# Kernel tuning notes

Hardware: AMD Instinct MI355X
Metric: run time of the kernel (lower is better)

Reference implementation:

```python
import jax, jax.numpy as jnp
import numpy as np
from jax import lax

B, DIM, H, W = 8, 256, 48, 48
HEADS, DH = 8, 32
K, S = 5, 2
P = K // 2
SCALE = DH ** -0.5
EPS = 1e-5


def setup_inputs() -> dict:
    key = jax.random.key(0)
    ks = jax.random.split(key, 12)
    w = lambda k, sh: jax.random.normal(k, sh, jnp.float32) * 0.02
    return {
        'x': jax.random.normal(ks[0], (B, DIM, H, W), jnp.float32),
        'kv': jax.random.normal(ks[1], (B, DIM, H, W), jnp.float32),
        'wq': w(ks[2], (DIM, DIM)), 'bq': jnp.zeros((DIM,), jnp.float32),
        'wk': w(ks[3], (DIM, DIM)), 'bk': jnp.zeros((DIM,), jnp.float32),
        'wv': w(ks[4], (DIM, DIM)), 'bv': jnp.zeros((DIM,), jnp.float32),
        'w_dw': w(ks[5], (DH, 1, K, K)), 'b_dw': jnp.zeros((DH,), jnp.float32),
        'ln_w': jnp.ones((DH,), jnp.float32), 'ln_b': jnp.zeros((DH,), jnp.float32),
        'w_off': w(ks[6], (2, DH)),
        'wo': w(ks[7], (DIM, DIM)), 'bo': jnp.zeros((DIM,), jnp.float32),
    }


def conv1x1(x, w, b=None):
    # x: (B, Cin, H, W), w: (Cout, Cin)
    y = jnp.einsum('oc,bchw->bohw', w, x)
    return y if b is None else y + b[None, :, None, None]


def grid_sample_bilinear(inp, grid):
    # inp: (N, C, Hh, Ww); grid: (N, Hg, Wg, 2) in (x, y), align_corners=True
    N, C, Hh, Ww = inp.shape
    gx = (grid[..., 0] + 1.0) * 0.5 * (Ww - 1)
    gy = (grid[..., 1] + 1.0) * 0.5 * (Hh - 1)
    x0 = jnp.floor(gx)
    y0 = jnp.floor(gy)
    wx = gx - x0  # frac weights for x1/y1 corners
    wy = gy - y0
    x0i = jnp.clip(x0.astype(jnp.int32), 0, Ww - 1)
    x1i = jnp.clip(x0.astype(jnp.int32) + 1, 0, Ww - 1)
    y0i = jnp.clip(y0.astype(jnp.int32), 0, Hh - 1)
    y1i = jnp.clip(y0.astype(jnp.int32) + 1, 0, Hh - 1)
    flat = inp.reshape(N, C, Hh * Ww)
    n = grid.shape[1] * grid.shape[2]

    def gather(yi, xi):
        idx = (yi * Ww + xi).reshape(N, 1, n)
        return jnp.take_along_axis(flat, jnp.broadcast_to(idx, (N, C, n)), axis=2)

    w00 = ((1 - wx) * (1 - wy)).reshape(N, 1, n)
    w01 = (wx * (1 - wy)).reshape(N, 1, n)
    w10 = ((1 - wx) * wy).reshape(N, 1, n)
    w11 = (wx * wy).reshape(N, 1, n)
    return (w00 * gather(y0i, x0i) + w01 * gather(y0i, x1i)
            + w10 * gather(y1i, x0i) + w11 * gather(y1i, x1i))  # (N, C, n)


def reference(x, kv, wq, bq, wk, bk, wv, bv, w_dw, b_dw, ln_w, ln_b, w_off, wo, bo):
    q = conv1x1(x, wq, bq)                      # (B, DIM, H, W)
    q_off = q.reshape(B * HEADS, DH, H, W)      # per-head channels
    # depthwise offset conv
    t = lax.conv_general_dilated(q_off, w_dw, (S, S), [(P, P), (P, P)],
                                 feature_group_count=DH,
                                 dimension_numbers=('NCHW', 'OIHW', 'NCHW'))
    t = t + b_dw[None, :, None, None]
    Hk, Wk = t.shape[2], t.shape[3]
    n = Hk * Wk
    # LayerNormProxy: LN over channel dim
    t = t.transpose(0, 2, 3, 1)                 # (BH, Hk, Wk, DH)
    mu = t.mean(-1, keepdims=True)
    var = ((t - mu) ** 2).mean(-1, keepdims=True)
    t = (t - mu) / jnp.sqrt(var + EPS) * ln_w + ln_b
    t = jax.nn.gelu(t, approximate=False)
    offset = jnp.einsum('oc,bhwc->bhwo', w_off, t)  # (BH, Hk, Wk, 2) as (y, x)
    # reference points, normalized to [-1, 1]
    ref_y = (jnp.linspace(0.5, Hk - 0.5, Hk, dtype=jnp.float32) / (Hk - 1.0)) * 2.0 - 1.0
    ref_x = (jnp.linspace(0.5, Wk - 0.5, Wk, dtype=jnp.float32) / (Wk - 1.0)) * 2.0 - 1.0
    ref = jnp.stack(jnp.meshgrid(ref_y, ref_x, indexing='ij'), axis=-1)  # (Hk, Wk, 2)
    pos = jnp.clip(offset + ref[None], -1.0, 1.0)
    grid = pos[..., ::-1]                       # (x, y) order for sampling
    kvs = grid_sample_bilinear(kv.reshape(B * HEADS, DH, H, W), grid)  # (BH, DH, n)
    kv4 = kvs.reshape(B, DIM, 1, n)
    k = conv1x1(kv4, wk, bk).reshape(B * HEADS, DH, n)
    v = conv1x1(kv4, wv, bv).reshape(B * HEADS, DH, n)
    qf = q.reshape(B * HEADS, DH, H * W)
    attn = jax.nn.softmax(jnp.einsum('bcm,bcn->bmn', qf, k) * SCALE, axis=2)
    out = jnp.einsum('bmn,bcn->bcm', attn, v).reshape(B, DIM, H, W)
    return conv1x1(out, wo, bo)
```

## Files before the change

kernel.cpp:

```cpp
#include <hip/hip_runtime.h>
#include <hip/hip_bf16.h>
#include <cstddef>

#define BB 8
#define DIM 256
#define HH 48
#define WW 48
#define HW 2304
#define HEADS 8
#define DH 32
#define BH 64
#define HK 24
#define WK 24
#define NN 576
#define SCALE 0.17677669529663687f
#define EPSF 1e-5f

typedef __attribute__((ext_vector_type(8))) short short8;
typedef __attribute__((ext_vector_type(4))) float f32x4;

static __device__ inline short f2bf_s(float f) {
  __hip_bfloat16 h = __float2bfloat16(f);
  return *reinterpret_cast<short*>(&h);
}

static __device__ inline unsigned pkrnd(float a, float b) {
  unsigned ua = __builtin_bit_cast(unsigned, a) + 0x8000u;
  unsigned ub = __builtin_bit_cast(unsigned, b) + 0x8000u;
  return __builtin_amdgcn_perm(ub, ua, 0x07060302);
}

__global__ __launch_bounds__(256) void prep(
    const float* __restrict__ x, const float* __restrict__ wq,
    short* __restrict__ Xh, short* __restrict__ Xl,
    short* __restrict__ Wqh, short* __restrict__ Wql) {
  __shared__ float t[64][65];
  const int bid = blockIdx.x;
  if (bid < 1152) {
    int mt = bid % 36, t2 = bid / 36;
    int ct = t2 & 3, b = t2 >> 2;
    const int c0 = ct * 64, m0 = mt * 64;
    const int col = threadIdx.x & 63, row4 = threadIdx.x >> 6;
    const float* xb = x + ((size_t)b * 256 + c0) * HW + m0;
#pragma unroll
    for (int k = 0; k < 16; k++) {
      int c = row4 + k * 4;
      t[c][col] = xb[(size_t)c * HW + col];
    }
    __syncthreads();
    short* oh = Xh + ((size_t)b * HW + m0) * 256 + c0;
    short* ol = Xl + ((size_t)b * HW + m0) * 256 + c0;
#pragma unroll
    for (int k = 0; k < 16; k++) {
      int m = row4 + k * 4;
      float v = t[col][m];
      unsigned u = __builtin_bit_cast(unsigned, v) & 0xffff0000u;
      float rem = v - __builtin_bit_cast(float, u);
      oh[(size_t)m * 256 + col] = (short)(u >> 16);
      ol[(size_t)m * 256 + col] = (short)(__builtin_bit_cast(unsigned, rem) >> 16);
    }
  } else {
    int e0 = (bid - 1152) * 1024 + threadIdx.x * 4;
    float4 v4 = *(const float4*)(wq + e0);
    float vv[4] = {v4.x, v4.y, v4.z, v4.w};
    union { short s[4]; int2 i2; } Hu, Lu;
#pragma unroll
    for (int j = 0; j < 4; j++) {
      unsigned u = __builtin_bit_cast(unsigned, vv[j]) & 0xffff0000u;
      float rem = vv[j] - __builtin_bit_cast(float, u);
      Hu.s[j] = (short)(u >> 16);
      Lu.s[j] = (short)(__builtin_bit_cast(unsigned, rem) >> 16);
    }
    *(int2*)(Wqh + e0) = Hu.i2;
    *(int2*)(Wql + e0) = Lu.i2;
  }
}

__global__ __launch_bounds__(512) void gemm_q_fused(
    const short* __restrict__ Wh, const short* __restrict__ Wl,
    const float* __restrict__ bias,
    const short* __restrict__ Xh, const short* __restrict__ Xl,
    float* __restrict__ Y,
    const float* __restrict__ kv, float* __restrict__ kvT,
    const float* __restrict__ wk, const float* __restrict__ wv,
    const float* __restrict__ wo,
    short* __restrict__ Wkh, short* __restrict__ Wkl,
    short* __restrict__ Wvh, short* __restrict__ Wvl,
    short* __restrict__ Woh, short* __restrict__ Wol) {
  __shared__ short sB[2][64 * 256];
  const int bid = blockIdx.x;
  const int tid = threadIdx.x;

  if (bid < 288) {
    const int b = bid / 36;
    const int mBase = (bid % 36) * 64;
    const short* srcH = Xh + ((size_t)b * HW + mBase) * 256;
    const short* srcL = Xl + ((size_t)b * HW + mBase) * 256;
#pragma unroll
    for (int it = 0; it < 4; it++) {
      int idx = it * 512 + tid;
      int row = idx >> 5, ck = idx & 31;
      int dst = row * 256 + ((ck ^ (row & 7)) << 3);
      *(short8*)(&sB[0][dst]) = *(const short8*)(srcH + (size_t)row * 256 + ck * 8);
      *(short8*)(&sB[1][dst]) = *(const short8*)(srcL + (size_t)row * 256 + ck * 8);
    }
    __syncthreads();

    const int wave = tid >> 6, lane = tid & 63;
    const int quad = lane >> 4, l15 = lane & 15;
    const int oBase = wave * 32;
    f32x4 acc[2][4] = {};
    for (int kc = 0; kc < 256; kc += 32) {
      short8 ah[2], al[2];
#pragma unroll
      for (int os = 0; os < 2; os++) {
        ah[os] = *(const short8*)(Wh + (size_t)(oBase + os * 16 + l15) * 256 + kc + quad * 8);
        al[os] = *(const short8*)(Wl + (size_t)(oBase + os * 16 + l15) * 256 + kc + quad * 8);
      }
#pragma unroll
      for (int mt = 0; mt < 4; mt++) {
        int row = mt * 16 + l15;
        int off = row * 256 + ((((kc >> 3) + quad) ^ (row & 7)) << 3);
        short8 bh_ = *(const short8*)(&sB[0][off]);
        short8 bl_ = *(const short8*)(&sB[1][off]);
#pragma unroll
        for (int os = 0; os < 2; os++) {
          acc[os][mt] = __builtin_amdgcn_mfma_f32_16x16x32_bf16(ah[os], bh_, acc[os][mt], 0, 0, 0);
          acc[os][mt] = __builtin_amdgcn_mfma_f32_16x16x32_bf16(al[os], bh_, acc[os][mt], 0, 0, 0);
          acc[os][mt] = __builtin_amdgcn_mfma_f32_16x16x32_bf16(ah[os], bl_, acc[os][mt], 0, 0, 0);
        }
      }
    }
#pragma unroll
    for (int os = 0; os < 2; os++)
#pragma unroll
      for (int r = 0; r < 4; r++) {
        int o = oBase + os * 16 + quad * 4 + r;
        float bs = bias[o];
        float* yp = Y + ((size_t)b * 256 + o) * HW + mBase + l15;
#pragma unroll
        for (int mt = 0; mt < 4; mt++) yp[mt * 16] = acc[os][mt][r] + bs;
      }
  } else if (bid < 1440) {
    float* tf = (float*)sB;
    int bb = bid - 288;
    int mt = bb % 36, t2 = bb / 36;
    int ct = t2 & 3, b = t2 >> 2;
    const int c0 = ct * 64, m0 = mt * 64;
    const int col = tid & 63, row8 = tid >> 6;
    const float* xb = kv + ((size_t)b * 256 + c0) * HW + m0;
#pragma unroll
    for (int k = 0; k < 8; k++) {
      int c = row8 + k * 8;
      tf[c * 65 + col] = xb[(size_t)c * HW + col];
    }
    __syncthreads();
    float* ot = kvT + ((size_t)b * HW + m0) * 256 + c0;
#pragma unroll
    for (int k = 0; k < 8; k++) {
      int m = row8 + k * 8;
      ot[(size_t)m * 256 + col] = tf[col * 65 + m];
    }
  } else {
    const float* srcs[3] = {wk, wv, wo};
    short* his[3] = {Wkh, Wvh, Woh};
    short* los[3] = {Wkl, Wvl, Wol};
    int bb = bid - 1440;
    int w = bb >> 5;
    int off = (bb & 31) * 2048 + tid * 4;
    float4 v4 = *(const float4*)(srcs[w] + off);
    float vv[4] = {v4.x, v4.y, v4.z, v4.w};
    union { short s[4]; int2 i2; } Hu, Lu;
#pragma unroll
    for (int j = 0; j < 4; j++) {
      unsigned u = __builtin_bit_cast(unsigned, vv[j]) & 0xffff0000u;
      float rem = vv[j] - __builtin_bit_cast(float, u);
      Hu.s[j] = (short)(u >> 16);
      Lu.s[j] = (short)(__builtin_bit_cast(unsigned, rem) >> 16);
    }
    *(int2*)(his[w] + off) = Hu.i2;
    *(int2*)(los[w] + off) = Lu.i2;
  }
}

#define QPS 101
__global__ __launch_bounds__(256) void dw_sample_kernel(
    const float* __restrict__ q, const float* __restrict__ kvT,
    const float* __restrict__ w_dw, const float* __restrict__ b_dw,
    const float* __restrict__ ln_w, const float* __restrict__ ln_b,
    const float* __restrict__ w_off, short* __restrict__ kvsTh,
    short* __restrict__ kvsTl) {
  __shared__ float s_q[32 * QPS];
  __shared__ float s_w[DH * 25];
  const int tid = threadIdx.x;
  const int ch = tid & 31;
  const int np = tid >> 5;
  const int bid = blockIdx.x;
  const int b = bid & 7;
  const int r = bid >> 3;
  const int head = r / 72;
  const int rr = r - head * 72;
  const int yk = rr / 3;
  const int xk0 = (rr - yk * 3) * 8;
  const int bh = b * 8 + head;
  const int xk = xk0 + np;
  const int n = yk * WK + xk;

  for (int i = tid; i < DH * 25; i += 256) s_w[i] = w_dw[i];

  {
    const int y0 = yk * 2 - 2, x0 = xk0 * 2 - 2;
    const float* qbh = q + (size_t)bh * DH * HW;
#pragma unroll
    for (int it = 0; it < 13; it++) {
      int e = it * 256 + tid;
      if (e < 3200) {
        int c = e / 100;
        int rem = e - c * 100;
        int dy = rem / 20;
        int xl = rem - dy * 20;
        int gy = y0 + dy, gx = x0 + xl;
        float v = 0.f;
        if ((unsigned)gy < HH && (unsigned)gx < WW)
          v = qbh[(size_t)c * HW + gy * WW + gx];
        s_q[c * QPS + dy * 20 + xl] = v;
      }
    }
  }
  __syncthreads();

  float t = b_dw[ch];
  {
    const float* wp = s_w + ch * 25;
    const float* qp = s_q + ch * QPS + np * 2;
#pragma unroll
    for (int dy = 0; dy < 5; dy++)
#pragma unroll
      for (int dx = 0; dx < 5; dx++)
        t += wp[dy * 5 + dx] * qp[dy * 20 + dx];
  }

  float mu = t;
#pragma unroll
  for (int m = 1; m < 32; m <<= 1) mu += __shfl_xor(mu, m);
  mu *= (1.0f / DH);
  float d = t - mu;
  float var = d * d;
#pragma unroll
  for (int m = 1; m < 32; m <<= 1) var += __shfl_xor(var, m);
  var *= (1.0f / DH);
  float rstd = rsqrtf(var + EPSF);

  float xn = d * rstd * ln_w[ch] + ln_b[ch];
  float g = 0.5f * xn * (1.0f + erff(xn * 0.70710678118654752f));
  float o0 = w_off[ch] * g;
  float o1 = w_off[DH + ch] * g;
#pragma unroll
  for (int m = 1; m < 32; m <<= 1) {
    o0 += __shfl_xor(o0, m);
    o1 += __shfl_xor(o1, m);
  }

  const float ref_y = (0.5f + (float)yk) / 23.0f * 2.0f - 1.0f;
  const float ref_x = (0.5f + (float)xk) / 23.0f * 2.0f - 1.0f;
  float py = fminf(fmaxf(o0 + ref_y, -1.0f), 1.0f);
  float px = fminf(fmaxf(o1 + ref_x, -1.0f), 1.0f);

  float gx = (px + 1.0f) * 0.5f * 47.0f;
  float gy = (py + 1.0f) * 0.5f * 47.0f;
  float x0f = floorf(gx), y0f = floorf(gy);
  float wx = gx - x0f, wy = gy - y0f;
  int x0 = (int)x0f, y0 = (int)y0f;
  int x0i = min(max(x0, 0), WW - 1);
  int x1i = min(max(x0 + 1, 0), WW - 1);
  int y0i = min(max(y0, 0), HH - 1);
  int y1i = min(max(y0 + 1, 0), HH - 1);
  float w00 = (1.f - wx) * (1.f - wy);
  float w01 = wx * (1.f - wy);
  float w10 = (1.f - wx) * wy;
  float w11 = wx * wy;

  const float* kvb = kvT + (size_t)b * HW * 256 + head * DH + ch;
  float val = w00 * kvb[(size_t)(y0i * WW + x0i) * 256]
            + w01 * kvb[(size_t)(y0i * WW + x1i) * 256]
            + w10 * kvb[(size_t)(y1i * WW + x0i) * 256]
            + w11 * kvb[(size_t)(y1i * WW + x1i) * 256];

  unsigned ub = __builtin_bit_cast(unsigned, val);
  unsigned uh = ub & 0xffff0000u;
  float rem = val - __builtin_bit_cast(float, uh);
  size_t idx = ((size_t)b * NN + n) * 256 + head * DH + ch;
  kvsTh[idx] = (short)(uh >> 16);
  kvsTl[idx] = (short)(__builtin_bit_cast(unsigned, rem) >> 16);
}

__global__ __launch_bounds__(256) void kv_gemm_mfma(
    const short* __restrict__ Wkh, const short* __restrict__ Wkl,
    const float* __restrict__ bk,
    const short* __restrict__ Wvh, const short* __restrict__ Wvl,
    const float* __restrict__ bv,
    const short* __restrict__ Xh, const short* __restrict__ Xl,
    short* __restrict__ Kb, short* __restrict__ Vb) {
  const int tid = threadIdx.x;
  const int wave = tid >> 6;
  const int lane = tid & 63;
  const int quad = lane >> 4, l15 = lane & 15;
  const int b = blockIdx.z;
  const int mode = blockIdx.y >> 2;
  const int oTile = (blockIdx.y & 3) * 64;
  const int nBase = blockIdx.x * 64;

  if (mode == 0) {
    const int nW = nBase + wave * 16;
    const short* arh = Xh + ((size_t)b * NN + nW + l15) * 256 + quad * 8;
    const short* arl = Xl + ((size_t)b * NN + nW + l15) * 256 + quad * 8;
    f32x4 acc[4] = {};
    for (int kc = 0; kc < 256; kc += 32) {
      short8 ah = *(const short8*)(arh + kc);
      short8 al = *(const short8*)(arl + kc);
#pragma unroll
      for (int ot = 0; ot < 4; ot++) {
        short8 bh_ = *(const short8*)(Wkh + (size_t)(oTile + ot * 16 + l15) * 256 + kc + quad * 8);
        short8 bl_ = *(const short8*)(Wkl + (size_t)(oTile + ot * 16 + l15) * 256 + kc + quad * 8);
        acc[ot] = __builtin_amdgcn_mfma_f32_16x16x32_bf16(ah, bh_, acc[ot], 0, 0, 0);
        acc[ot] = __builtin_amdgcn_mfma_f32_16x16x32_bf16(al, bh_, acc[ot], 0, 0, 0);
        acc[ot] = __builtin_amdgcn_mfma_f32_16x16x32_bf16(ah, bl_, acc[ot], 0, 0, 0);
      }
    }
    float bs[4];
#pragma unroll
    for (int ot = 0; ot < 4; ot++) bs[ot] = bk[oTile + ot * 16 + l15];
#pragma unroll
    for (int r = 0; r < 4; r++) {
      short* yp = Kb + ((size_t)b * NN + nW + quad * 4 + r) * 256 + oTile + l15;
#pragma unroll
      for (int ot = 0; ot < 4; ot++) yp[ot * 16] = f2bf_s(acc[ot][r] + bs[ot]);
    }
  } else {
    const int oW = oTile + wave * 16;
    const short* arh = Wvh + (size_t)(oW + l15) * 256 + quad * 8;
    const short* arl = Wvl + (size_t)(oW + l15) * 256 + quad * 8;
    f32x4 acc[4] = {};
    for (int kc = 0; kc < 256; kc += 32) {
      short8 ah = *(const short8*)(arh + kc);
      short8 al = *(const short8*)(arl + kc);
#pragma unroll
      for (int nt = 0; nt < 4; nt++) {
        short8 bh_ = *(const short8*)(Xh + ((size_t)b * NN + nBase + nt * 16 + l15) * 256 + kc + quad * 8);
        short8 bl_ = *(const short8*)(Xl + ((size_t)b * NN + nBase + nt * 16 + l15) * 256 + kc + quad * 8);
        acc[nt] = __builtin_amdgcn_mfma_f32_16x16x32_bf16(ah, bh_, acc[nt], 0, 0, 0);
        acc[nt] = __builtin_amdgcn_mfma_f32_16x16x32_bf16(al, bh_, acc[nt], 0, 0, 0);
        acc[nt] = __builtin_amdgcn_mfma_f32_16x16x32_bf16(ah, bl_, acc[nt], 0, 0, 0);
      }
    }
#pragma unroll
    for (int r = 0; r < 4; r++) {
      int o = oW + quad * 4 + r;
      float bs = bv[o];
      short* yp = Vb + ((size_t)b * 256 + o) * NN + nBase + l15;
#pragma unroll
      for (int nt = 0; nt < 4; nt++) yp[nt * 16] = f2bf_s(acc[nt][r] + bs);
    }
  }
}

__global__ __launch_bounds__(256) void attn_mfma(const float* __restrict__ q,
                                                 const short* __restrict__ Kb,
                                                 const short* __restrict__ Vb,
                                                 short* __restrict__ O) {
  __shared__ short sK[2][64 * 40];
  __shared__ short sV[2][32 * 88];
  __shared__ int sP[4][2][256];
  const int tid = threadIdx.x;
  const int wave = tid >> 6;
  const int lane = tid & 63;
  const int quad = lane >> 4;
  const int l15 = lane & 15;
  const int bh = blockIdx.y;
  const int b = bh >> 3, head = bh & 7;
  const int mBase = blockIdx.x * 128 + wave * 32;

  short8 bq[2];
#pragma unroll
  for (int mt = 0; mt < 2; mt++) {
    const float* qp = q + ((size_t)bh * DH + quad * 8) * HW + mBase + mt * 16 + l15;
    short8 v;
#pragma unroll
    for (int j = 0; j < 8; j++) v[j] = f2bf_s(qp[(size_t)j * HW] * SCALE);
    bq[mt] = v;
  }

  const int kn = tid >> 2, kc = (tid & 3) * 8;
  const int vc = tid >> 3, vn = (tid & 7) * 8;
  const short* kg = Kb + (size_t)b * NN * 256 + head * DH;
  const short* vg = Vb + ((size_t)b * 256 + head * DH) * NN;

  short8 kreg = *(const short8*)(kg + (size_t)kn * 256 + kc);
  short8 vreg = *(const short8*)(vg + (size_t)vc * NN + vn);
  *(short8*)(&sK[0][kn * 40 + kc]) = kreg;
  *(short8*)(&sV[0][vc * 88 + vn]) = vreg;
  __syncthreads();

  const int g = (l15 >> 1) & 3;
  const int row16 = l15 * 16;
  const int wr0 = row16 + (((quad >> 1) ^ g) << 2) + ((quad & 1) << 1);
  const int wr1 = row16 + (((2 + (quad >> 1)) ^ g) << 2) + ((quad & 1) << 1);
  const int rd = row16 + ((quad ^ g) << 2);

  f32x4 oacc[2][2] = {};
  f32x4 dacc[2] = {};
  const short ONE = 0x3F80;
  const short8 ones = {ONE, ONE, ONE, ONE, ONE, ONE, ONE, ONE};

  for (int s = 0; s < 9; s++) {
    const int buf = s & 1;
    if (s + 1 < 9) {
      kreg = *(const short8*)(kg + (size_t)((s + 1) * 64 + kn) * 256 + kc);
      vreg = *(const short8*)(vg + (size_t)vc * NN + (s + 1) * 64 + vn);
    }
#pragma unroll
    for (int nt = 0; nt < 2; nt++) {
      short8 ka0 = *(const short8*)(&sK[buf][(nt * 32 + l15) * 40 + quad * 8]);
      short8 ka1 = *(const short8*)(&sK[buf][(nt * 32 + 16 + l15) * 40 + quad * 8]);
      short8 va0 = *(const short8*)(&sV[buf][l15 * 88 + nt * 32 + quad * 8]);
      short8 va1 = *(const short8*)(&sV[buf][(16 + l15) * 88 + nt * 32 + quad * 8]);
      f32x4 z = {0.f, 0.f, 0.f, 0.f};
      f32x4 st[2][2];
      st[0][0] = __builtin_amdgcn_mfma_f32_16x16x32_bf16(ka0, bq[0], z, 0, 0, 0);
      st[0][1] = __builtin_amdgcn_mfma_f32_16x16x32_bf16(ka1, bq[0], z, 0, 0, 0);
      st[1][0] = __builtin_amdgcn_mfma_f32_16x16x32_bf16(ka0, bq[1], z, 0, 0, 0);
      st[1][1] = __builtin_amdgcn_mfma_f32_16x16x32_bf16(ka1, bq[1], z, 0, 0, 0);
#pragma unroll
      for (int mt = 0; mt < 2; mt++) {
        float p0 = __expf(st[mt][0][0]), p1 = __expf(st[mt][0][1]);
        float p2 = __expf(st[mt][0][2]), p3 = __expf(st[mt][0][3]);
        float p4 = __expf(st[mt][1][0]), p5 = __expf(st[mt][1][1]);
        float p6 = __expf(st[mt][1][2]), p7 = __expf(st[mt][1][3]);
        int* base = &sP[wave][mt][0];
        *(int2*)(base + wr0) = make_int2((int)pkrnd(p0, p1), (int)pkrnd(p2, p3));
        *(int2*)(base + wr1) = make_int2((int)pkrnd(p4, p5), (int)pkrnd(p6, p7));
      }
#pragma unroll
      for (int mt = 0; mt < 2; mt++) {
        short8 pa = *(short8*)(&sP[wave][mt][0] + rd);
        oacc[mt][0] = __builtin_amdgcn_mfma_f32_16x16x32_bf16(pa, va0, oacc[mt][0], 0, 0, 0);
        oacc[mt][1] = __builtin_amdgcn_mfma_f32_16x16x32_bf16(pa, va1, oacc[mt][1], 0, 0, 0);
        dacc[mt] = __builtin_amdgcn_mfma_f32_16x16x32_bf16(pa, ones, dacc[mt], 0, 0, 0);
      }
    }
    if (s + 1 < 9) {
      *(short8*)(&sK[buf ^ 1][kn * 40 + kc]) = kreg;
      *(short8*)(&sV[buf ^ 1][vc * 88 + vn]) = vreg;
    }
    __syncthreads();
  }

#pragma unroll
  for (int mt = 0; mt < 2; mt++) {
    short* ob = O + ((size_t)b * HW + mBase + mt * 16) * 256 + head * DH + l15;
#pragma unroll
    for (int r = 0; r < 4; r++) {
      float inv = 1.0f / dacc[mt][r];
      ob[(size_t)(quad * 4 + r) * 256] = f2bf_s(oacc[mt][0][r] * inv);
      ob[(size_t)(quad * 4 + r) * 256 + 16] = f2bf_s(oacc[mt][1][r] * inv);
    }
  }
}

__global__ __launch_bounds__(512) void wo_gemm_mfma(const short* __restrict__ Whi,
                                                    const short* __restrict__ Wlo,
                                                    const float* __restrict__ bias,
                                                    const short* __restrict__ X,
                                                    float* __restrict__ Y) {
  __shared__ short sX[64 * 256];
  const int tid = threadIdx.x;
  const int b = blockIdx.y;
  const int mBase = blockIdx.x * 64;

  const short* src = X + ((size_t)b * HW + mBase) * 256;
#pragma unroll
  for (int it = 0; it < 4; it++) {
    int idx = it * 512 + tid;
    int row = idx >> 5, ck = idx & 31;
    *(short8*)(&sX[row * 256 + ((ck ^ (row & 7)) << 3)]) =
        *(const short8*)(src + (size_t)row * 256 + ck * 8);
  }
  __syncthreads();

  const int wave = tid >> 6, lane = tid & 63;
  const int quad = lane >> 4, l15 = lane & 15;
  const int oBase = wave * 32;

  f32x4 acc[2][4] = {};
  for (int kc = 0; kc < 256; kc += 32) {
    short8 ah[2], al[2];
#pragma unroll
    for (int os = 0; os < 2; os++) {
      ah[os] = *(const short8*)(Whi + (size_t)(oBase + os * 16 + l15) * 256 + kc + quad * 8);
      al[os] = *(const short8*)(Wlo + (size_t)(oBase + os * 16 + l15) * 256 + kc + quad * 8);
    }
#pragma unroll
    for (int mt = 0; mt < 4; mt++) {
      int row = mt * 16 + l15;
      short8 bx = *(const short8*)(&sX[row * 256 + ((((kc >> 3) + quad) ^ (row & 7)) << 3)]);
#pragma unroll
      for (int os = 0; os < 2; os++) {
        acc[os][mt] = __builtin_amdgcn_mfma_f32_16x16x32_bf16(ah[os], bx, acc[os][mt], 0, 0, 0);
        acc[os][mt] = __builtin_amdgcn_mfma_f32_16x16x32_bf16(al[os], bx, acc[os][mt], 0, 0, 0);
      }
    }
  }

#pragma unroll
  for (int os = 0; os < 2; os++)
#pragma unroll
    for (int r = 0; r < 4; r++) {
      int o = oBase + os * 16 + quad * 4 + r;
      float bs = bias[o];
      float* yp = Y + ((size_t)b * 256 + o) * HW + mBase + l15;
#pragma unroll
      for (int mt = 0; mt < 4; mt++) yp[mt * 16] = acc[os][mt][r] + bs;
    }
}

extern "C" void kernel_launch(void* const* d_in, const int* in_sizes, int n_in,
                              void* d_out, int out_size, void* d_ws, size_t ws_size,
                              hipStream_t stream) {
  const float* x    = (const float*)d_in[0];
  const float* kv   = (const float*)d_in[1];
  const float* wq   = (const float*)d_in[2];
  const float* bq   = (const float*)d_in[3];
  const float* wk   = (const float*)d_in[4];
  const float* bk   = (const float*)d_in[5];
  const float* wv   = (const float*)d_in[6];
  const float* bv   = (const float*)d_in[7];
  const float* w_dw = (const float*)d_in[8];
  const float* b_dw = (const float*)d_in[9];
  const float* ln_w = (const float*)d_in[10];
  const float* ln_b = (const float*)d_in[11];
  const float* w_off= (const float*)d_in[12];
  const float* wo   = (const float*)d_in[13];
  const float* bo   = (const float*)d_in[14];
  float* out = (float*)d_out;
  float* ws = (float*)d_ws;

  float* q     = ws;
  short* Xth   = (short*)(ws + 4718592);
  short* O     = (short*)(ws + 4718592);
  short* Xtl   = (short*)(ws + 7077888);
  short* kvsTh = (short*)(ws + 7077888);
  short* kvsTl = (short*)(ws + 7667712);
  short* Kb    = (short*)(ws + 8257536);
  short* Vb    = (short*)(ws + 8847360);
  short* Wqh   = (short*)(ws + 9437184);
  short* Wql = Wqh + 65536;
  short* Wkh = Wql + 65536;
  short* Wkl = Wkh + 65536;
  short* Wvh = Wkl + 65536;
  short* Wvl = Wvh + 65536;
  short* Woh = Wvl + 65536;
  short* Wol = Woh + 65536;
  float* kvT = out;

  prep<<<dim3(1216), dim3(256), 0, stream>>>(x, wq, Xth, Xtl, Wqh, Wql);
  gemm_q_fused<<<dim3(1536), dim3(512), 0, stream>>>(
      Wqh, Wql, bq, Xth, Xtl, q,
      kv, kvT, wk, wv, wo, Wkh, Wkl, Wvh, Wvl, Woh, Wol);
  dw_sample_kernel<<<dim3(BH * NN / 8), dim3(256), 0, stream>>>(
      q, kvT, w_dw, b_dw, ln_w, ln_b, w_off, kvsTh, kvsTl);
  kv_gemm_mfma<<<dim3(NN / 64, 8, BB), dim3(256), 0, stream>>>(
      Wkh, Wkl, bk, Wvh, Wvl, bv, kvsTh, kvsTl, Kb, Vb);
  attn_mfma<<<dim3(HW / 128, BH), dim3(256), 0, stream>>>(q, Kb, Vb, O);
  wo_gemm_mfma<<<dim3(HW / 64, BB), dim3(512), 0, stream>>>(Woh, Wol, bo, O, out);
}
```

Baseline: 230.7 us.

## Retile Q/Wo GEMMs, emit pre-scaled bf16 Q, add MFMA priority hints

The Q-projection and output GEMMs now use 256-thread blocks over 32-row tiles, with each wave covering 64 output channels. This doubles the block count and is meant to improve occupancy and reuse of the weight fragments. The Q GEMM epilogue also writes a head-major, scale-folded bf16 copy of Q, so attention loads its Q fragments with two vector loads instead of strided fp32 reads and per-element conversion. The attention kernel wraps its MFMA groups in s_setprio, and the transpose and weight-split branches are remapped to the new block size. The cost is an extra bf16 Q buffer write and more per-wave accumulator registers.

```diff
diff --git a/kernel.cpp b/kernel.cpp
--- a/kernel.cpp
+++ b/kernel.cpp
@@ -76,29 +76,29 @@
   }
 }
 
-__global__ __launch_bounds__(512) void gemm_q_fused(
+__global__ __launch_bounds__(256) void gemm_q_fused(
     const short* __restrict__ Wh, const short* __restrict__ Wl,
     const float* __restrict__ bias,
     const short* __restrict__ Xh, const short* __restrict__ Xl,
-    float* __restrict__ Y,
+    float* __restrict__ Y, short* __restrict__ Qbf,
     const float* __restrict__ kv, float* __restrict__ kvT,
     const float* __restrict__ wk, const float* __restrict__ wv,
     const float* __restrict__ wo,
     short* __restrict__ Wkh, short* __restrict__ Wkl,
     short* __restrict__ Wvh, short* __restrict__ Wvl,
     short* __restrict__ Woh, short* __restrict__ Wol) {
-  __shared__ short sB[2][64 * 256];
+  __shared__ short sB[2][32 * 256];
   const int bid = blockIdx.x;
   const int tid = threadIdx.x;
 
-  if (bid < 288) {
-    const int b = bid / 36;
-    const int mBase = (bid % 36) * 64;
+  if (bid < 576) {
+    const int b = bid & 7;
+    const int mBase = (bid >> 3) * 32;
     const short* srcH = Xh + ((size_t)b * HW + mBase) * 256;
     const short* srcL = Xl + ((size_t)b * HW + mBase) * 256;
 #pragma unroll
     for (int it = 0; it < 4; it++) {
-      int idx = it * 512 + tid;
+      int idx = it * 256 + tid;
       int row = idx >> 5, ck = idx & 31;
       int dst = row * 256 + ((ck ^ (row & 7)) << 3);
       *(short8*)(&sB[0][dst]) = *(const short8*)(srcH + (size_t)row * 256 + ck * 8);
@@ -108,23 +108,23 @@
 
     const int wave = tid >> 6, lane = tid & 63;
     const int quad = lane >> 4, l15 = lane & 15;
-    const int oBase = wave * 32;
-    f32x4 acc[2][4] = {};
+    const int oBase = wave * 64;
+    f32x4 acc[4][2] = {};
     for (int kc = 0; kc < 256; kc += 32) {
-      short8 ah[2], al[2];
-#pragma unroll
-      for (int os = 0; os < 2; os++) {
+      short8 ah[4], al[4];
+#pragma unroll
+      for (int os = 0; os < 4; os++) {
         ah[os] = *(const short8*)(Wh + (size_t)(oBase + os * 16 + l15) * 256 + kc + quad * 8);
         al[os] = *(const short8*)(Wl + (size_t)(oBase + os * 16 + l15) * 256 + kc + quad * 8);
       }
 #pragma unroll
-      for (int mt = 0; mt < 4; mt++) {
+      for (int mt = 0; mt < 2; mt++) {
         int row = mt * 16 + l15;
         int off = row * 256 + ((((kc >> 3) + quad) ^ (row & 7)) << 3);
         short8 bh_ = *(const short8*)(&sB[0][off]);
         short8 bl_ = *(const short8*)(&sB[1][off]);
 #pragma unroll
-        for (int os = 0; os < 2; os++) {
+        for (int os = 0; os < 4; os++) {
           acc[os][mt] = __builtin_amdgcn_mfma_f32_16x16x32_bf16(ah[os], bh_, acc[os][mt], 0, 0, 0);
           acc[os][mt] = __builtin_amdgcn_mfma_f32_16x16x32_bf16(al[os], bh_, acc[os][mt], 0, 0, 0);
           acc[os][mt] = __builtin_amdgcn_mfma_f32_16x16x32_bf16(ah[os], bl_, acc[os][mt], 0, 0, 0);
@@ -132,42 +132,48 @@
       }
     }
 #pragma unroll
-    for (int os = 0; os < 2; os++)
+    for (int os = 0; os < 4; os++)
 #pragma unroll
       for (int r = 0; r < 4; r++) {
         int o = oBase + os * 16 + quad * 4 + r;
         float bs = bias[o];
+        int head = o >> 5, c = o & 31;
         float* yp = Y + ((size_t)b * 256 + o) * HW + mBase + l15;
-#pragma unroll
-        for (int mt = 0; mt < 4; mt++) yp[mt * 16] = acc[os][mt][r] + bs;
-      }
-  } else if (bid < 1440) {
+        short* qp = Qbf + ((size_t)(b * 8 + head) * HW + mBase + l15) * 32 + c;
+#pragma unroll
+        for (int mt = 0; mt < 2; mt++) {
+          float v = acc[os][mt][r] + bs;
+          yp[mt * 16] = v;
+          qp[mt * 16 * 32] = f2bf_s(v * SCALE);
+        }
+      }
+  } else if (bid < 1728) {
     float* tf = (float*)sB;
-    int bb = bid - 288;
+    int bb = bid - 576;
     int mt = bb % 36, t2 = bb / 36;
     int ct = t2 & 3, b = t2 >> 2;
     const int c0 = ct * 64, m0 = mt * 64;
-    const int col = tid & 63, row8 = tid >> 6;
+    const int col = tid & 63, row4 = tid >> 6;
     const float* xb = kv + ((size_t)b * 256 + c0) * HW + m0;
 #pragma unroll
-    for (int k = 0; k < 8; k++) {
-      int c = row8 + k * 8;
+    for (int k = 0; k < 16; k++) {
+      int c = row4 + k * 4;
       tf[c * 65 + col] = xb[(size_t)c * HW + col];
     }
     __syncthreads();
     float* ot = kvT + ((size_t)b * HW + m0) * 256 + c0;
 #pragma unroll
-    for (int k = 0; k < 8; k++) {
-      int m = row8 + k * 8;
+    for (int k = 0; k < 16; k++) {
+      int m = row4 + k * 4;
       ot[(size_t)m * 256 + col] = tf[col * 65 + m];
     }
   } else {
     const float* srcs[3] = {wk, wv, wo};
     short* his[3] = {Wkh, Wvh, Woh};
     short* los[3] = {Wkl, Wvl, Wol};
-    int bb = bid - 1440;
-    int w = bb >> 5;
-    int off = (bb & 31) * 2048 + tid * 4;
+    int bb = bid - 1728;
+    int w = bb >> 6;
+    int off = (bb & 63) * 1024 + tid * 4;
     float4 v4 = *(const float4*)(srcs[w] + off);
     float vv[4] = {v4.x, v4.y, v4.z, v4.w};
     union { short s[4]; int2 i2; } Hu, Lu;
@@ -364,7 +370,7 @@
   }
 }
 
-__global__ __launch_bounds__(256) void attn_mfma(const float* __restrict__ q,
+__global__ __launch_bounds__(256) void attn_mfma(const short* __restrict__ Qbf,
                                                  const short* __restrict__ Kb,
                                                  const short* __restrict__ Vb,
                                                  short* __restrict__ O) {
@@ -381,13 +387,10 @@
   const int mBase = blockIdx.x * 128 + wave * 32;
 
   short8 bq[2];
-#pragma unroll
-  for (int mt = 0; mt < 2; mt++) {
-    const float* qp = q + ((size_t)bh * DH + quad * 8) * HW + mBase + mt * 16 + l15;
-    short8 v;
-#pragma unroll
-    for (int j = 0; j < 8; j++) v[j] = f2bf_s(qp[(size_t)j * HW] * SCALE);
-    bq[mt] = v;
+  {
+    const short* qbp = Qbf + ((size_t)bh * HW + mBase + l15) * 32 + quad * 8;
+    bq[0] = *(const short8*)(qbp);
+    bq[1] = *(const short8*)(qbp + 16 * 32);
   }
 
   const int kn = tid >> 2, kc = (tid & 3) * 8;
@@ -426,10 +429,12 @@
       short8 va1 = *(const short8*)(&sV[buf][(16 + l15) * 88 + nt * 32 + quad * 8]);
       f32x4 z = {0.f, 0.f, 0.f, 0.f};
       f32x4 st[2][2];
+      __builtin_amdgcn_s_setprio(1);
       st[0][0] = __builtin_amdgcn_mfma_f32_16x16x32_bf16(ka0, bq[0], z, 0, 0, 0);
       st[0][1] = __builtin_amdgcn_mfma_f32_16x16x32_bf16(ka1, bq[0], z, 0, 0, 0);
       st[1][0] = __builtin_amdgcn_mfma_f32_16x16x32_bf16(ka0, bq[1], z, 0, 0, 0);
       st[1][1] = __builtin_amdgcn_mfma_f32_16x16x32_bf16(ka1, bq[1], z, 0, 0, 0);
+      __builtin_amdgcn_s_setprio(0);
 #pragma unroll
       for (int mt = 0; mt < 2; mt++) {
         float p0 = __expf(st[mt][0][0]), p1 = __expf(st[mt][0][1]);
@@ -443,9 +448,11 @@
 #pragma unroll
       for (int mt = 0; mt < 2; mt++) {
         short8 pa = *(short8*)(&sP[wave][mt][0] + rd);
+        __builtin_amdgcn_s_setprio(1);
         oacc[mt][0] = __builtin_amdgcn_mfma_f32_16x16x32_bf16(pa, va0, oacc[mt][0], 0, 0, 0);
         oacc[mt][1] = __builtin_amdgcn_mfma_f32_16x16x32_bf16(pa, va1, oacc[mt][1], 0, 0, 0);
         dacc[mt] = __builtin_amdgcn_mfma_f32_16x16x32_bf16(pa, ones, dacc[mt], 0, 0, 0);
+        __builtin_amdgcn_s_setprio(0);
       }
     }
     if (s + 1 < 9) {
@@ -467,20 +474,21 @@
   }
 }
 
-__global__ __launch_bounds__(512) void wo_gemm_mfma(const short* __restrict__ Whi,
+__global__ __launch_bounds__(256) void wo_gemm_mfma(const short* __restrict__ Whi,
                                                     const short* __restrict__ Wlo,
                                                     const float* __restrict__ bias,
                                                     const short* __restrict__ X,
                                                     float* __restrict__ Y) {
-  __shared__ short sX[64 * 256];
+  __shared__ short sX[32 * 256];
   const int tid = threadIdx.x;
-  const int b = blockIdx.y;
-  const int mBase = blockIdx.x * 64;
+  const int bid = blockIdx.x;
+  const int b = bid & 7;
+  const int mBase = (bid >> 3) * 32;
 
   const short* src = X + ((size_t)b * HW + mBase) * 256;
 #pragma unroll
   for (int it = 0; it < 4; it++) {
-    int idx = it * 512 + tid;
+    int idx = it * 256 + tid;
     int row = idx >> 5, ck = idx & 31;
     *(short8*)(&sX[row * 256 + ((ck ^ (row & 7)) << 3)]) =
         *(const short8*)(src + (size_t)row * 256 + ck * 8);
@@ -489,22 +497,22 @@
 
   const int wave = tid >> 6, lane = tid & 63;
   const int quad = lane >> 4, l15 = lane & 15;
-  const int oBase = wave * 32;
-
-  f32x4 acc[2][4] = {};
+  const int oBase = wave * 64;
+
+  f32x4 acc[4][2] = {};
   for (int kc = 0; kc < 256; kc += 32) {
-    short8 ah[2], al[2];
-#pragma unroll
-    for (int os = 0; os < 2; os++) {
+    short8 ah[4], al[4];
+#pragma unroll
+    for (int os = 0; os < 4; os++) {
       ah[os] = *(const short8*)(Whi + (size_t)(oBase + os * 16 + l15) * 256 + kc + quad * 8);
       al[os] = *(const short8*)(Wlo + (size_t)(oBase + os * 16 + l15) * 256 + kc + quad * 8);
     }
 #pragma unroll
-    for (int mt = 0; mt < 4; mt++) {
+    for (int mt = 0; mt < 2; mt++) {
       int row = mt * 16 + l15;
       short8 bx = *(const short8*)(&sX[row * 256 + ((((kc >> 3) + quad) ^ (row & 7)) << 3)]);
 #pragma unroll
-      for (int os = 0; os < 2; os++) {
+      for (int os = 0; os < 4; os++) {
         acc[os][mt] = __builtin_amdgcn_mfma_f32_16x16x32_bf16(ah[os], bx, acc[os][mt], 0, 0, 0);
         acc[os][mt] = __builtin_amdgcn_mfma_f32_16x16x32_bf16(al[os], bx, acc[os][mt], 0, 0, 0);
       }
@@ -512,14 +520,14 @@
   }
 
 #pragma unroll
-  for (int os = 0; os < 2; os++)
+  for (int os = 0; os < 4; os++)
 #pragma unroll
     for (int r = 0; r < 4; r++) {
       int o = oBase + os * 16 + quad * 4 + r;
       float bs = bias[o];
       float* yp = Y + ((size_t)b * 256 + o) * HW + mBase + l15;
 #pragma unroll
-      for (int mt = 0; mt < 4; mt++) yp[mt * 16] = acc[os][mt][r] + bs;
+      for (int mt = 0; mt < 2; mt++) yp[mt * 16] = acc[os][mt][r] + bs;
     }
 }
 
@@ -560,16 +568,17 @@
   short* Wvl = Wvh + 65536;
   short* Woh = Wvl + 65536;
   short* Wol = Woh + 65536;
+  short* Qbf = (short*)(ws + 9699328);
   float* kvT = out;
 
   prep<<<dim3(1216), dim3(256), 0, stream>>>(x, wq, Xth, Xtl, Wqh, Wql);
-  gemm_q_fused<<<dim3(1536), dim3(512), 0, stream>>>(
-      Wqh, Wql, bq, Xth, Xtl, q,
+  gemm_q_fused<<<dim3(1920), dim3(256), 0, stream>>>(
+      Wqh, Wql, bq, Xth, Xtl, q, Qbf,
       kv, kvT, wk, wv, wo, Wkh, Wkl, Wvh, Wvl, Woh, Wol);
   dw_sample_kernel<<<dim3(BH * NN / 8), dim3(256), 0, stream>>>(
       q, kvT, w_dw, b_dw, ln_w, ln_b, w_off, kvsTh, kvsTl);
   kv_gemm_mfma<<<dim3(NN / 64, 8, BB), dim3(256), 0, stream>>>(
       Wkh, Wkl, bk, Wvh, Wvl, bv, kvsTh, kvsTl, Kb, Vb);
-  attn_mfma<<<dim3(HW / 128, BH), dim3(256), 0, stream>>>(q, Kb, Vb, O);
-  wo_gemm_mfma<<<dim3(HW / 64, BB), dim3(512), 0, stream>>>(Woh, Wol, bo, O, out);
-}
+  attn_mfma<<<dim3(HW / 128, BH), dim3(256), 0, stream>>>(Qbf, Kb, Vb, O);
+  wo_gemm_mfma<<<dim3(576), dim3(256), 0, stream>>>(Woh, Wol, bo, O, out);
+}
```

After: 253.2 us. 1.1x slower.
